# Optimization experiments

Measured on AMD Instinct MI355X. Metric: run time of the kernel, lower is better.

Reference implementation:

```python
import jax, jax.numpy as jnp
import numpy as np

BETA = 0.25


def setup_inputs() -> dict:
    key = jax.random.key(0)
    k1, k2 = jax.random.split(key)
    z_e = jax.random.normal(k1, (16, 256, 2048), dtype=jnp.float32)   # [B, C, L]
    # nn.Embedding weight initialized uniform(-1, 1): [num_codewords, codebook_dim]
    emb = jax.random.uniform(k2, (2048, 256), dtype=jnp.float32, minval=-1.0, maxval=1.0)
    return {"z_e": z_e, "emb": emb}


def reference(z_e, emb):
    C = emb.shape[1]
    # Faithful to the torch code: permute(2,1,0) -> [L, C, B], then view(-1, C)
    z = jnp.transpose(z_e, (2, 1, 0))          # [L, C, B]
    flat = z.reshape(-1, C)                    # [N, C] where N = L*C*B / C
    d = (jnp.sum(flat * flat, axis=1, keepdims=True)
         + jnp.sum(emb * emb, axis=1)
         - 2.0 * flat @ emb.T)                 # [N, K]
    indices = jnp.argmin(d, axis=1)            # [N]
    quantized = emb[indices].reshape(z.shape)  # [L, C, B]
    sg = jax.lax.stop_gradient
    vq_loss = (jnp.mean((sg(quantized) - z) ** 2)
               + BETA * jnp.mean((quantized - sg(z)) ** 2))
    return quantized, indices, vq_loss
```

## Files before the change

kernel.cpp:

```cpp
#include <hip/hip_runtime.h>


#define ZE_CL   (256 * 2048)
#define NROWS   32768
#define KC      2048
#define DD      256
#define IDX_OFF 8388608
#define LOSS_OFF (8388608 + 32768)
#define D2 8e-3f

typedef __bf16 bf16x4 __attribute__((ext_vector_type(4)));
typedef __bf16 bf16x8 __attribute__((ext_vector_type(8)));
typedef float  f32x4  __attribute__((ext_vector_type(4)));

#define EN_OFF  0u
#define EH_OFF  8192u
#define EL_OFF  (EH_OFF + 1048576u)
#define AH_OFF  (EL_OFF + 1048576u)
#define AL_OFF  (AH_OFF + 16777216u)
#define CNT_OFF (AL_OFF + 16777216u)
#define LST_OFF (CNT_OFF + 16u)
#define WS_NEED (LST_OFF + 131072u)

static __device__ inline void gld_lds16(const void* g, void* l) {
    __builtin_amdgcn_global_load_lds(
        (const __attribute__((address_space(1))) void*)g,
        (__attribute__((address_space(3))) void*)l, 16, 0, 0);
}

__global__ void vq_prep_all(const float* __restrict__ ze, const float* __restrict__ emb,
                            float* __restrict__ out, float* __restrict__ enorm,
                            __bf16* __restrict__ Eh, __bf16* __restrict__ El,
                            __bf16* __restrict__ Ah, __bf16* __restrict__ Al,
                            int* __restrict__ rcount) {
    __shared__ float T[16 * 272];
    int tid = threadIdx.x;
    int bid = blockIdx.x;

    if (bid >= 2048) {
        int pb = bid - 2048;
        if (pb == 0) {
            if (tid < 4) rcount[tid] = 0;
            if (tid == 4) out[LOSS_OFF] = 0.f;
        }
        int col = pb * 32 + (tid >> 3);
        int ch  = tid & 7;
        const float4* src = (const float4*)(emb + (size_t)col * DD);
        int t8 = col >> 8, g = (col >> 4) & 15, c = col & 15;
        float s = 0.f;
#pragma unroll
        for (int q = 0; q < 4; ++q) {
            float4 v0 = src[ch * 8 + q * 2];
            float4 v1 = src[ch * 8 + q * 2 + 1];
            float f[8] = {v0.x, v0.y, v0.z, v0.w, v1.x, v1.y, v1.z, v1.w};
            bf16x8 h, l;
#pragma unroll
            for (int j = 0; j < 8; ++j) {
                h[j] = (__bf16)f[j];
                l[j] = (__bf16)(f[j] - (float)h[j]);
                s += f[j] * f[j];
            }
            size_t off = ((size_t)(t8 * 8 + ch) * 16384) + (size_t)(g * 1024 + q * 256 + c * 16);
            *(bf16x8*)((char*)Eh + off) = h;
            *(bf16x8*)((char*)El + off) = l;
        }
        s += __shfl_xor(s, 1, 64);
        s += __shfl_xor(s, 2, 64);
        s += __shfl_xor(s, 4, 64);
        if (ch == 0) enorm[col] = s;
        return;
    }

    float* A = out;
    int m  = bid & 15;
    int lt = bid >> 4;
    int l0 = lt * 16;
#pragma unroll
    for (int it = 0; it < 4; ++it) {
        int p   = tid + it * 256;
        int b   = p >> 6;
        int clo = (p >> 2) & 15;
        int l4  = p & 3;
        const float* g = ze + (size_t)b * ZE_CL + (size_t)(m * 16 + clo) * 2048 + l0 + 4 * l4;
        float4 v = *(const float4*)g;
        int jp = 17 * clo + b;
        T[(4 * l4 + 0) * 272 + jp] = v.x;
        T[(4 * l4 + 1) * 272 + jp] = v.y;
        T[(4 * l4 + 2) * 272 + jp] = v.z;
        T[(4 * l4 + 3) * 272 + jp] = v.w;
    }
    __syncthreads();
#pragma unroll
    for (int it = 0; it < 4; ++it) {
        int p  = tid + it * 256;
        int ll = p >> 6;
        int c4 = p & 63;
        int j0 = 4 * c4;
        int base = ll * 272 + 17 * (j0 >> 4) + (j0 & 15);
        float4 v;
        v.x = T[base + 0]; v.y = T[base + 1]; v.z = T[base + 2]; v.w = T[base + 3];
        int n = (l0 + ll) * 16 + m;
        *(float4*)(A + (size_t)n * DD + j0) = v;
        {
            float a0 = -2.f * v.x, a1 = -2.f * v.y, a2 = -2.f * v.z, a3 = -2.f * v.w;
            bf16x4 h, l;
            h[0] = (__bf16)a0; l[0] = (__bf16)(a0 - (float)h[0]);
            h[1] = (__bf16)a1; l[1] = (__bf16)(a1 - (float)h[1]);
            h[2] = (__bf16)a2; l[2] = (__bf16)(a2 - (float)h[2]);
            h[3] = (__bf16)a3; l[3] = (__bf16)(a3 - (float)h[3]);
            int bn = n >> 6, mi = (n >> 4) & 3, r = n & 15;
            int ch = j0 >> 5, q = (j0 >> 3) & 3, hb = (j0 & 7) * 2;
            size_t off = (size_t)bn * 32768 + (size_t)((mi * 8 + ch) * 1024 + q * 256 + r * 16 + hb);
            *(bf16x4*)((char*)Ah + off) = h;
            *(bf16x4*)((char*)Al + off) = l;
        }
    }
}

__global__ __launch_bounds__(256, 2) void vq_main_mfma(
    const __bf16* __restrict__ Ah, const __bf16* __restrict__ Al,
    const __bf16* __restrict__ Eh, const __bf16* __restrict__ El,
    const float* __restrict__ enorm, const float* __restrict__ emb,
    float* out, int* __restrict__ rcount, int* __restrict__ rlist)
{
    __shared__ __align__(16) char sA[32768];
    float* sRv   = (float*)sA;
    float* sR2   = (float*)(sA + 512);
    int*   sRi   = (int*)(sA + 1024);
    int*   sIdx  = (int*)(sA + 1536);
    int*   sFlag = (int*)(sA + 1664);
    float* wsum  = (float*)(sA + 1792);

    const int tid  = threadIdx.x;
    const int wv   = tid >> 6;
    const int lane = tid & 63;
    const int l15  = lane & 15;
    const int quad = lane >> 4;
    const int n0   = blockIdx.x * 32;
    const int bn   = blockIdx.x >> 1;
    const int miB  = (blockIdx.x & 1) * 2;
    const int nt0  = (blockIdx.x >> 3) & 7;
    const int ch0  = (blockIdx.x >> 6) & 7;

    {
        const char* srcH = (const char*)Ah + (size_t)bn * 32768 + (size_t)miB * 8192;
        const char* srcL = (const char*)Al + (size_t)bn * 32768 + (size_t)miB * 8192;
#pragma unroll
        for (int it = 0; it < 4; ++it) {
            int off = (it * 4 + wv) * 1024;
            gld_lds16(srcH + off + lane * 16, sA + off);
            gld_lds16(srcL + off + lane * 16, sA + 16384 + off);
        }
    }

    const char* EhW = (const char*)Eh + (size_t)(wv * 4) * 1024 + (size_t)lane * 16;
    const char* ElW = (const char*)El + (size_t)(wv * 4) * 1024 + (size_t)lane * 16;
    const char* sAl16 = sA + (size_t)lane * 16;

    float v1[8], v2[8]; int i1[8];
#pragma unroll
    for (int s = 0; s < 8; ++s) { v1[s] = 3.4e38f; v2[s] = 3.4e38f; i1[s] = 0; }

    __syncthreads();

    for (int ntc = 0; ntc < 8; ++ntc) {
        int nt = ntc + nt0; if (nt >= 8) nt -= 8;
        const char* EhT = EhW + (size_t)nt * 131072;
        const char* ElT = ElW + (size_t)nt * 131072;
        f32x4 acc[2][4];
#pragma unroll
        for (int a = 0; a < 2; ++a)
#pragma unroll
            for (int b = 0; b < 4; ++b) acc[a][b] = (f32x4){0.f, 0.f, 0.f, 0.f};

#pragma unroll 2
        for (int chc = 0; chc < 8; ++chc) {
            int ch = chc + ch0; if (ch >= 8) ch -= 8;
            bf16x8 ah[2], al[2], bh[4], bl[4];
#pragma unroll
            for (int nj = 0; nj < 4; ++nj) {
                size_t boff = (size_t)(ch * 16384 + nj * 1024);
                bh[nj] = *(const bf16x8*)(EhT + boff);
                bl[nj] = *(const bf16x8*)(ElT + boff);
            }
#pragma unroll
            for (int mi = 0; mi < 2; ++mi) {
                size_t off = (size_t)((mi * 8 + ch) * 1024);
                ah[mi] = *(const bf16x8*)(sAl16 + off);
                al[mi] = *(const bf16x8*)(sAl16 + 16384 + off);
            }
#pragma unroll
            for (int mi = 0; mi < 2; ++mi)
#pragma unroll
                for (int nj = 0; nj < 4; ++nj)
                    acc[mi][nj] = __builtin_amdgcn_mfma_f32_16x16x32_bf16(ah[mi], bh[nj], acc[mi][nj], 0, 0, 0);
#pragma unroll
            for (int mi = 0; mi < 2; ++mi)
#pragma unroll
                for (int nj = 0; nj < 4; ++nj)
                    acc[mi][nj] = __builtin_amdgcn_mfma_f32_16x16x32_bf16(ah[mi], bl[nj], acc[mi][nj], 0, 0, 0);
#pragma unroll
            for (int mi = 0; mi < 2; ++mi)
#pragma unroll
                for (int nj = 0; nj < 4; ++nj)
                    acc[mi][nj] = __builtin_amdgcn_mfma_f32_16x16x32_bf16(al[mi], bh[nj], acc[mi][nj], 0, 0, 0);
        }
#pragma unroll
        for (int nj = 0; nj < 4; ++nj) {
            int k = nt * 256 + wv * 64 + nj * 16 + l15;
            float en = enorm[k];
#pragma unroll
            for (int mi = 0; mi < 2; ++mi)
#pragma unroll
                for (int r = 0; r < 4; ++r) {
                    float d = acc[mi][nj][r] + en;
                    int slot = mi * 4 + r;
                    float nv2 = fminf(v2[slot], fmaxf(v1[slot], d));
                    if (d < v1[slot]) i1[slot] = k;
                    v1[slot] = fminf(v1[slot], d);
                    v2[slot] = nv2;
                }
        }
    }

    __syncthreads();

#pragma unroll
    for (int slot = 0; slot < 8; ++slot) {
        float a1 = v1[slot], a2 = v2[slot];
        int ai = i1[slot];
#pragma unroll
        for (int m = 1; m < 16; m <<= 1) {
            float b1 = __shfl_xor(a1, m, 64);
            float b2 = __shfl_xor(a2, m, 64);
            int bi = __shfl_xor(ai, m, 64);
            float n2 = fminf(fminf(a2, b2), fmaxf(a1, b1));
            if (b1 < a1) ai = bi;
            a1 = fminf(a1, b1);
            a2 = n2;
        }
        if (l15 == 0) {
            int row = (slot >> 2) * 16 + quad * 4 + (slot & 3);
            sRv[row * 4 + wv] = a1;
            sR2[row * 4 + wv] = a2;
            sRi[row * 4 + wv] = ai;
        }
    }
    __syncthreads();
    if (tid < 32) {
        float a1 = sRv[tid * 4], a2 = sR2[tid * 4];
        int ai = sRi[tid * 4];
#pragma unroll
        for (int w2 = 1; w2 < 4; ++w2) {
            float b1 = sRv[tid * 4 + w2], b2 = sR2[tid * 4 + w2];
            int bi = sRi[tid * 4 + w2];
            float n2 = fminf(fminf(a2, b2), fmaxf(a1, b1));
            if (b1 < a1) ai = bi;
            a1 = fminf(a1, b1);
            a2 = n2;
        }
        int fg = (a2 - a1 < D2) ? 1 : 0;
        sIdx[tid] = ai;
        sFlag[tid] = fg;
        out[IDX_OFF + n0 + tid] = (float)ai;
        if (fg) { int p = atomicAdd(rcount, 1); rlist[p] = n0 + tid; }
    }
    __syncthreads();

    float lacc = 0.f;
#pragma unroll
    for (int it = 0; it < 8; ++it) {
        int p = tid + it * 256;
        int r = p >> 6;
        int c4 = p & 63;
        if (!sFlag[r]) {
            int k = sIdx[r];
            size_t off = (size_t)(n0 + r) * DD + 4 * c4;
            float4 q = *(const float4*)(emb + (size_t)k * DD + 4 * c4);
            float4 a = *(const float4*)(out + off);
            float dx = q.x - a.x, dy = q.y - a.y, dz = q.z - a.z, dw = q.w - a.w;
            lacc += dx * dx + dy * dy + dz * dz + dw * dw;
            *(float4*)(out + off) = q;
        }
    }
#pragma unroll
    for (int off = 32; off > 0; off >>= 1) lacc += __shfl_down(lacc, off, 64);
    if ((tid & 63) == 0) wsum[tid >> 6] = lacc;
    __syncthreads();
    if (tid == 0) {
        float bs = wsum[0] + wsum[1] + wsum[2] + wsum[3];
        atomicAdd(out + LOSS_OFF, bs * (1.25f / 8388608.0f));
    }
}

__global__ void vq_rescore(const float* __restrict__ emb, const float* __restrict__ enorm,
                           float* out, const int* __restrict__ rcount,
                           const int* __restrict__ rlist) {
    __shared__ float sX[256];
    __shared__ float sV[256];
    __shared__ int   sK[256];
    __shared__ float sP[256];
    int cnt = *rcount;
    int tid = threadIdx.x;
    for (int li = blockIdx.x; li < cnt; li += gridDim.x) {
        int row = rlist[li];
        __syncthreads();
        sX[tid] = out[(size_t)row * DD + tid];
        __syncthreads();
        float bv = 3.4e38f; int bk = 0;
        for (int jj = 0; jj < 8; ++jj) {
            int k = jj * 256 + tid;
            const float4* e4 = (const float4*)(emb + (size_t)k * DD);
            float dot = 0.f;
#pragma unroll 8
            for (int d4 = 0; d4 < 64; ++d4) {
                float4 e = e4[d4];
                float4 x = *(const float4*)(sX + d4 * 4);
                dot += x.x * e.x + x.y * e.y + x.z * e.z + x.w * e.w;
            }
            float s = enorm[k] - 2.f * dot;
            if (s < bv) { bv = s; bk = k; }
        }
        sV[tid] = bv; sK[tid] = bk;
        __syncthreads();
#pragma unroll
        for (int s = 128; s > 0; s >>= 1) {
            if (tid < s) {
                float vo = sV[tid + s]; int ko = sK[tid + s];
                if (vo < sV[tid] || (vo == sV[tid] && ko < sK[tid])) { sV[tid] = vo; sK[tid] = ko; }
            }
            __syncthreads();
        }
        int k = sK[0];
        float x = sX[tid];
        float q = emb[(size_t)k * DD + tid];
        out[(size_t)row * DD + tid] = q;
        float d = q - x;
        sP[tid] = d * d;
        __syncthreads();
#pragma unroll
        for (int s = 128; s > 0; s >>= 1) {
            if (tid < s) sP[tid] += sP[tid + s];
            __syncthreads();
        }
        if (tid == 0) {
            out[IDX_OFF + row] = (float)k;
            atomicAdd(out + LOSS_OFF, sP[0] * (1.25f / 8388608.0f));
        }
    }
}

__global__ void vq_prep_emb(const float* __restrict__ emb, float* __restrict__ enorm,
                            __bf16* __restrict__ Eh, __bf16* __restrict__ El) {
    int tid = threadIdx.x;
    int col = blockIdx.x * 32 + (tid >> 3);
    int ch  = tid & 7;
    const float4* src = (const float4*)(emb + (size_t)col * DD);
    int t8 = col >> 8, g = (col >> 4) & 15, c = col & 15;
    float s = 0.f;
#pragma unroll
    for (int q = 0; q < 4; ++q) {
        float4 v0 = src[ch * 8 + q * 2];
        float4 v1 = src[ch * 8 + q * 2 + 1];
        float f[8] = {v0.x, v0.y, v0.z, v0.w, v1.x, v1.y, v1.z, v1.w};
        bf16x8 h, l;
#pragma unroll
        for (int j = 0; j < 8; ++j) {
            h[j] = (__bf16)f[j];
            l[j] = (__bf16)(f[j] - (float)h[j]);
            s += f[j] * f[j];
        }
        size_t off = ((size_t)(t8 * 8 + ch) * 16384) + (size_t)(g * 1024 + q * 256 + c * 16);
        *(bf16x8*)((char*)Eh + off) = h;
        *(bf16x8*)((char*)El + off) = l;
    }
    s += __shfl_xor(s, 1, 64);
    s += __shfl_xor(s, 2, 64);
    s += __shfl_xor(s, 4, 64);
    if (ch == 0) enorm[col] = s;
}

__global__ void vq_transpose_split(const float* __restrict__ ze, float* __restrict__ A,
                                   __bf16* __restrict__ Ah, __bf16* __restrict__ Al) {
    __shared__ float T[16 * 272];
    int tid = threadIdx.x;
    int m  = blockIdx.x & 15;
    int lt = blockIdx.x >> 4;
    int l0 = lt * 16;
#pragma unroll
    for (int it = 0; it < 4; ++it) {
        int p   = tid + it * 256;
        int b   = p >> 6;
        int clo = (p >> 2) & 15;
        int l4  = p & 3;
        const float* g = ze + (size_t)b * ZE_CL + (size_t)(m * 16 + clo) * 2048 + l0 + 4 * l4;
        float4 v = *(const float4*)g;
        int jp = 17 * clo + b;
        T[(4 * l4 + 0) * 272 + jp] = v.x;
        T[(4 * l4 + 1) * 272 + jp] = v.y;
        T[(4 * l4 + 2) * 272 + jp] = v.z;
        T[(4 * l4 + 3) * 272 + jp] = v.w;
    }
    __syncthreads();
#pragma unroll
    for (int it = 0; it < 4; ++it) {
        int p  = tid + it * 256;
        int ll = p >> 6;
        int c4 = p & 63;
        int j0 = 4 * c4;
        int base = ll * 272 + 17 * (j0 >> 4) + (j0 & 15);
        float4 v;
        v.x = T[base + 0]; v.y = T[base + 1]; v.z = T[base + 2]; v.w = T[base + 3];
        int n = (l0 + ll) * 16 + m;
        *(float4*)(A + (size_t)n * DD + j0) = v;
        if (Ah) {
            float a0 = -2.f * v.x, a1 = -2.f * v.y, a2 = -2.f * v.z, a3 = -2.f * v.w;
            bf16x4 h, l;
            h[0] = (__bf16)a0; l[0] = (__bf16)(a0 - (float)h[0]);
            h[1] = (__bf16)a1; l[1] = (__bf16)(a1 - (float)h[1]);
            h[2] = (__bf16)a2; l[2] = (__bf16)(a2 - (float)h[2]);
            h[3] = (__bf16)a3; l[3] = (__bf16)(a3 - (float)h[3]);
            int bn = n >> 6, mi = (n >> 4) & 3, r = n & 15;
            int ch = j0 >> 5, q = (j0 >> 3) & 3, hb = (j0 & 7) * 2;
            size_t off = (size_t)bn * 32768 + (size_t)((mi * 8 + ch) * 1024 + q * 256 + r * 16 + hb);
            *(bf16x4*)((char*)Ah + off) = h;
            *(bf16x4*)((char*)Al + off) = l;
        }
    }
}

__global__ __launch_bounds__(256, 2) void vq_main_f32(const float* __restrict__ emb,
                                                      const float* __restrict__ enorm,
                                                      float* out) {
    const int SA = 68, SE = 68;
    __shared__ float smem[64 * 68 + 64 * 68];
    __shared__ int   sIdx[64];
    __shared__ float wsum[4];
    float* sA = smem;
    float* sEb = smem + 64 * SA;
    float* redv = sEb;
    int*   redi = (int*)(sEb + 64 * 16);
    int tid = threadIdx.x;
    int n0 = blockIdx.x * 64;
    int rg = tid & 15;
    int kg = tid >> 4;
    float minv[4]; int mini[4];
#pragma unroll
    for (int i = 0; i < 4; ++i) { minv[i] = 3.4e38f; mini[i] = 0; }
    const float* A = out;
    for (int kt = 0; kt < KC / 64; ++kt) {
        int k0 = kt * 64;
        float acc[4][4];
#pragma unroll
        for (int i = 0; i < 4; ++i)
#pragma unroll
            for (int j = 0; j < 4; ++j) acc[i][j] = 0.f;
        for (int dc = 0; dc < 4; ++dc) {
            int d0 = dc * 64;
            __syncthreads();
#pragma unroll
            for (int it = 0; it < 4; ++it) {
                int p = tid + it * 256, r = p >> 4, c4 = p & 15;
                *(float4*)(sA + r * SA + 4 * c4) =
                    *(const float4*)(A + (size_t)(n0 + r) * DD + d0 + 4 * c4);
            }
#pragma unroll
            for (int it = 0; it < 4; ++it) {
                int p = tid + it * 256, r = p >> 4, c4 = p & 15;
                *(float4*)(sEb + r * SE + 4 * c4) =
                    *(const float4*)(emb + (size_t)(k0 + r) * DD + d0 + 4 * c4);
            }
            __syncthreads();
#pragma unroll
            for (int d4 = 0; d4 < 16; ++d4) {
                float4 av[4], ev[4];
#pragma unroll
                for (int i = 0; i < 4; ++i) av[i] = *(const float4*)(sA + (rg + 16 * i) * SA + 4 * d4);
#pragma unroll
                for (int j = 0; j < 4; ++j) ev[j] = *(const float4*)(sEb + (kg + 16 * j) * SE + 4 * d4);
#pragma unroll
                for (int i = 0; i < 4; ++i)
#pragma unroll
                    for (int j = 0; j < 4; ++j)
                        acc[i][j] += av[i].x * ev[j].x + av[i].y * ev[j].y +
                                     av[i].z * ev[j].z + av[i].w * ev[j].w;
            }
        }
#pragma unroll
        for (int j = 0; j < 4; ++j) {
            int k = k0 + kg + 16 * j;
            float en = enorm[k];
#pragma unroll
            for (int i = 0; i < 4; ++i) {
                float s = en - 2.f * acc[i][j];
                if (s < minv[i]) { minv[i] = s; mini[i] = k; }
            }
        }
    }
    __syncthreads();
#pragma unroll
    for (int i = 0; i < 4; ++i) {
        int r = rg + 16 * i;
        redv[r * 16 + kg] = minv[i];
        redi[r * 16 + kg] = mini[i];
    }
    __syncthreads();
    if (tid < 64) {
        float bv = redv[tid * 16]; int bi = redi[tid * 16];
        for (int t = 1; t < 16; ++t) {
            float v = redv[tid * 16 + t]; int ii = redi[tid * 16 + t];
            if (v < bv || (v == bv && ii < bi)) { bv = v; bi = ii; }
        }
        sIdx[tid] = bi;
        out[IDX_OFF + n0 + tid] = (float)bi;
    }
    __syncthreads();
    float lacc = 0.f;
#pragma unroll
    for (int it = 0; it < 16; ++it) {
        int p = tid + it * 256, r = p >> 6, c4 = p & 63;
        int k = sIdx[r];
        size_t off = (size_t)(n0 + r) * DD + 4 * c4;
        float4 q = *(const float4*)(emb + (size_t)k * DD + 4 * c4);
        float4 a = *(const float4*)(out + off);
        float dx = q.x - a.x, dy = q.y - a.y, dz = q.z - a.z, dw = q.w - a.w;
        lacc += dx * dx + dy * dy + dz * dz + dw * dw;
        *(float4*)(out + off) = q;
    }
#pragma unroll
    for (int off = 32; off > 0; off >>= 1) lacc += __shfl_down(lacc, off, 64);
    if ((tid & 63) == 0) wsum[tid >> 6] = lacc;
    __syncthreads();
    if (tid == 0) {
        float bs = wsum[0] + wsum[1] + wsum[2] + wsum[3];
        atomicAdd(out + LOSS_OFF, bs * (1.25f / 8388608.0f));
    }
}

extern "C" void kernel_launch(void* const* d_in, const int* in_sizes, int n_in,
                              void* d_out, int out_size, void* d_ws, size_t ws_size,
                              hipStream_t stream) {
    (void)in_sizes; (void)n_in; (void)out_size;
    const float* ze  = (const float*)d_in[0];
    const float* emb = (const float*)d_in[1];
    float* out = (float*)d_out;
    char*  ws  = (char*)d_ws;
    float* enorm = (float*)(ws + EN_OFF);

    if (ws_size >= (size_t)WS_NEED) {
        __bf16* Eh = (__bf16*)(ws + EH_OFF);
        __bf16* El = (__bf16*)(ws + EL_OFF);
        __bf16* Ah = (__bf16*)(ws + AH_OFF);
        __bf16* Al = (__bf16*)(ws + AL_OFF);
        int* rcount = (int*)(ws + CNT_OFF);
        int* rlist  = (int*)(ws + LST_OFF);
        vq_prep_all<<<2112, 256, 0, stream>>>(ze, emb, out, enorm, Eh, El, Ah, Al, rcount);
        vq_main_mfma<<<NROWS / 32, 256, 0, stream>>>(Ah, Al, Eh, El, enorm, emb, out, rcount, rlist);
        vq_rescore<<<512, 256, 0, stream>>>(emb, enorm, out, rcount, rlist);
    } else {
        hipMemsetAsync((char*)d_out + (size_t)LOSS_OFF * 4, 0, 4, stream);
        vq_prep_emb<<<64, 256, 0, stream>>>(emb, enorm, (__bf16*)(ws + EH_OFF), (__bf16*)(ws + EH_OFF));
        vq_transpose_split<<<2048, 256, 0, stream>>>(ze, out, (__bf16*)0, (__bf16*)0);
        vq_main_f32<<<NROWS / 64, 256, 0, stream>>>(emb, enorm, out);
    }
}
```

Baseline: 279.4 us.

## Fuse ambiguous-row fp32 rescoring into main MFMA kernel, drop separate rescore launch

Moves the exact fp32 rescoring of near-tie rows from a separate kernel into the tail of the main MFMA kernel. Each block rescans its own flagged rows, which removes the global atomic counter, the row list, one kernel launch and the zeroing of the counter. The change also drops the per-block rotation of the tile and channel start offsets and fully unrolls the channel loop. The risk is load imbalance: blocks with many flagged rows now serialize that work inside the main kernel instead of spreading it across a dedicated grid. Removing the start-offset rotation may also bring back cache or channel contention on the embedding reads.

After: 363.7 us. +30.2%, slower.

```diff
diff --git a/kernel.cpp b/kernel.cpp
--- a/kernel.cpp
+++ b/kernel.cpp
@@ -31,18 +31,14 @@
 __global__ void vq_prep_all(const float* __restrict__ ze, const float* __restrict__ emb,
                             float* __restrict__ out, float* __restrict__ enorm,
                             __bf16* __restrict__ Eh, __bf16* __restrict__ El,
-                            __bf16* __restrict__ Ah, __bf16* __restrict__ Al,
-                            int* __restrict__ rcount) {
+                            __bf16* __restrict__ Ah, __bf16* __restrict__ Al) {
     __shared__ float T[16 * 272];
     int tid = threadIdx.x;
     int bid = blockIdx.x;
 
     if (bid >= 2048) {
         int pb = bid - 2048;
-        if (pb == 0) {
-            if (tid < 4) rcount[tid] = 0;
-            if (tid == 4) out[LOSS_OFF] = 0.f;
-        }
+        if (pb == 0 && tid == 0) out[LOSS_OFF] = 0.f;
         int col = pb * 32 + (tid >> 3);
         int ch  = tid & 7;
         const float4* src = (const float4*)(emb + (size_t)col * DD);
@@ -121,7 +117,7 @@
     const __bf16* __restrict__ Ah, const __bf16* __restrict__ Al,
     const __bf16* __restrict__ Eh, const __bf16* __restrict__ El,
     const float* __restrict__ enorm, const float* __restrict__ emb,
-    float* out, int* __restrict__ rcount, int* __restrict__ rlist)
+    float* out)
 {
     __shared__ __align__(16) char sA[32768];
     float* sRv   = (float*)sA;
@@ -130,6 +126,10 @@
     int*   sIdx  = (int*)(sA + 1536);
     int*   sFlag = (int*)(sA + 1664);
     float* wsum  = (float*)(sA + 1792);
+    float* sX    = (float*)(sA + 4096);
+    float* sV    = (float*)(sA + 5120);
+    int*   sK    = (int*)(sA + 6144);
+    float* sP    = (float*)(sA + 7168);
 
     const int tid  = threadIdx.x;
     const int wv   = tid >> 6;
@@ -139,8 +139,6 @@
     const int n0   = blockIdx.x * 32;
     const int bn   = blockIdx.x >> 1;
     const int miB  = (blockIdx.x & 1) * 2;
-    const int nt0  = (blockIdx.x >> 3) & 7;
-    const int ch0  = (blockIdx.x >> 6) & 7;
 
     {
         const char* srcH = (const char*)Ah + (size_t)bn * 32768 + (size_t)miB * 8192;
@@ -163,8 +161,7 @@
 
     __syncthreads();
 
-    for (int ntc = 0; ntc < 8; ++ntc) {
-        int nt = ntc + nt0; if (nt >= 8) nt -= 8;
+    for (int nt = 0; nt < 8; ++nt) {
         const char* EhT = EhW + (size_t)nt * 131072;
         const char* ElT = ElW + (size_t)nt * 131072;
         f32x4 acc[2][4];
@@ -173,9 +170,8 @@
 #pragma unroll
             for (int b = 0; b < 4; ++b) acc[a][b] = (f32x4){0.f, 0.f, 0.f, 0.f};
 
-#pragma unroll 2
-        for (int chc = 0; chc < 8; ++chc) {
-            int ch = chc + ch0; if (ch >= 8) ch -= 8;
+#pragma unroll
+        for (int ch = 0; ch < 8; ++ch) {
             bf16x8 ah[2], al[2], bh[4], bl[4];
 #pragma unroll
             for (int nj = 0; nj < 4; ++nj) {
@@ -259,13 +255,59 @@
             a1 = fminf(a1, b1);
             a2 = n2;
         }
-        int fg = (a2 - a1 < D2) ? 1 : 0;
+        sFlag[tid] = (a2 - a1 < D2) ? 1 : 0;
         sIdx[tid] = ai;
-        sFlag[tid] = fg;
         out[IDX_OFF + n0 + tid] = (float)ai;
-        if (fg) { int p = atomicAdd(rcount, 1); rlist[p] = n0 + tid; }
-    }
-    __syncthreads();
+    }
+    __syncthreads();
+
+    for (int r = 0; r < 32; ++r) {
+        if (!sFlag[r]) continue;
+        int row = n0 + r;
+        sX[tid] = out[(size_t)row * DD + tid];
+        __syncthreads();
+        float bv = 3.4e38f; int bk = 0;
+        for (int jj = 0; jj < 8; ++jj) {
+            int k = jj * 256 + tid;
+            const float4* e4 = (const float4*)(emb + (size_t)k * DD);
+            float dot = 0.f;
+#pragma unroll 8
+            for (int d4 = 0; d4 < 64; ++d4) {
+                float4 e = e4[d4];
+                float4 x = *(const float4*)(sX + d4 * 4);
+                dot += x.x * e.x + x.y * e.y + x.z * e.z + x.w * e.w;
+            }
+            float s = enorm[k] - 2.f * dot;
+            if (s < bv) { bv = s; bk = k; }
+        }
+        sV[tid] = bv; sK[tid] = bk;
+        __syncthreads();
+#pragma unroll
+        for (int s = 128; s > 0; s >>= 1) {
+            if (tid < s) {
+                float vo = sV[tid + s]; int ko = sK[tid + s];
+                if (vo < sV[tid] || (vo == sV[tid] && ko < sK[tid])) { sV[tid] = vo; sK[tid] = ko; }
+            }
+            __syncthreads();
+        }
+        int k = sK[0];
+        float x = sX[tid];
+        float q = emb[(size_t)k * DD + tid];
+        out[(size_t)row * DD + tid] = q;
+        float d = q - x;
+        sP[tid] = d * d;
+        __syncthreads();
+#pragma unroll
+        for (int s = 128; s > 0; s >>= 1) {
+            if (tid < s) sP[tid] += sP[tid + s];
+            __syncthreads();
+        }
+        if (tid == 0) {
+            out[IDX_OFF + row] = (float)k;
+            atomicAdd(out + LOSS_OFF, sP[0] * (1.25f / 8388608.0f));
+        }
+        __syncthreads();
+    }
 
     float lacc = 0.f;
 #pragma unroll
@@ -290,63 +332,6 @@
     if (tid == 0) {
         float bs = wsum[0] + wsum[1] + wsum[2] + wsum[3];
         atomicAdd(out + LOSS_OFF, bs * (1.25f / 8388608.0f));
-    }
-}
-
-__global__ void vq_rescore(const float* __restrict__ emb, const float* __restrict__ enorm,
-                           float* out, const int* __restrict__ rcount,
-                           const int* __restrict__ rlist) {
-    __shared__ float sX[256];
-    __shared__ float sV[256];
-    __shared__ int   sK[256];
-    __shared__ float sP[256];
-    int cnt = *rcount;
-    int tid = threadIdx.x;
-    for (int li = blockIdx.x; li < cnt; li += gridDim.x) {
-        int row = rlist[li];
-        __syncthreads();
-        sX[tid] = out[(size_t)row * DD + tid];
-        __syncthreads();
-        float bv = 3.4e38f; int bk = 0;
-        for (int jj = 0; jj < 8; ++jj) {
-            int k = jj * 256 + tid;
-            const float4* e4 = (const float4*)(emb + (size_t)k * DD);
-            float dot = 0.f;
-#pragma unroll 8
-            for (int d4 = 0; d4 < 64; ++d4) {
-                float4 e = e4[d4];
-                float4 x = *(const float4*)(sX + d4 * 4);
-                dot += x.x * e.x + x.y * e.y + x.z * e.z + x.w * e.w;
-            }
-            float s = enorm[k] - 2.f * dot;
-            if (s < bv) { bv = s; bk = k; }
-        }
-        sV[tid] = bv; sK[tid] = bk;
-        __syncthreads();
-#pragma unroll
-        for (int s = 128; s > 0; s >>= 1) {
-            if (tid < s) {
-                float vo = sV[tid + s]; int ko = sK[tid + s];
-                if (vo < sV[tid] || (vo == sV[tid] && ko < sK[tid])) { sV[tid] = vo; sK[tid] = ko; }
-            }
-            __syncthreads();
-        }
-        int k = sK[0];
-        float x = sX[tid];
-        float q = emb[(size_t)k * DD + tid];
-        out[(size_t)row * DD + tid] = q;
-        float d = q - x;
-        sP[tid] = d * d;
-        __syncthreads();
-#pragma unroll
-        for (int s = 128; s > 0; s >>= 1) {
-            if (tid < s) sP[tid] += sP[tid + s];
-            __syncthreads();
-        }
-        if (tid == 0) {
-            out[IDX_OFF + row] = (float)k;
-            atomicAdd(out + LOSS_OFF, sP[0] * (1.25f / 8388608.0f));
-        }
     }
 }
 
@@ -552,11 +537,8 @@
         __bf16* El = (__bf16*)(ws + EL_OFF);
         __bf16* Ah = (__bf16*)(ws + AH_OFF);
         __bf16* Al = (__bf16*)(ws + AL_OFF);
-        int* rcount = (int*)(ws + CNT_OFF);
-        int* rlist  = (int*)(ws + LST_OFF);
-        vq_prep_all<<<2112, 256, 0, stream>>>(ze, emb, out, enorm, Eh, El, Ah, Al, rcount);
-        vq_main_mfma<<<NROWS / 32, 256, 0, stream>>>(Ah, Al, Eh, El, enorm, emb, out, rcount, rlist);
-        vq_rescore<<<512, 256, 0, stream>>>(emb, enorm, out, rcount, rlist);
+        vq_prep_all<<<2112, 256, 0, stream>>>(ze, emb, out, enorm, Eh, El, Ah, Al);
+        vq_main_mfma<<<NROWS / 32, 256, 0, stream>>>(Ah, Al, Eh, El, enorm, emb, out);
     } else {
         hipMemsetAsync((char*)d_out + (size_t)LOSS_OFF * 4, 0, 4, stream);
         vq_prep_emb<<<64, 256, 0, stream>>>(emb, enorm, (__bf16*)(ws + EH_OFF), (__bf16*)(ws + EH_OFF));
```
